# Optimization experiments

Measured on AMD Instinct MI355X. Metric: run time of the kernel, lower is better.

Reference implementation:

```python
import jax, jax.numpy as jnp
import numpy as np

HIDDEN = 2048
EXPERTS = 8
INTER = 1024
TOP_K = 2
AUX_LOSS_WEIGHT = 0.01
TOKENS = 8192


def setup_inputs() -> dict:
    key = jax.random.key(0)
    k_x, k_g, k_w1, k_w2 = jax.random.split(key, 4)
    x = jax.random.normal(k_x, (TOKENS, HIDDEN), dtype=jnp.float32)
    # nn.Linear(hidden, experts, bias=False): weight is [E, H], applied as x @ W^T
    gate_w = jax.random.normal(k_g, (EXPERTS, HIDDEN), dtype=jnp.float32) * 0.02
    w1 = jax.random.normal(k_w1, (EXPERTS, HIDDEN, INTER), dtype=jnp.float32) * 0.02
    w2 = jax.random.normal(k_w2, (EXPERTS, INTER, HIDDEN), dtype=jnp.float32) * 0.02
    return {"x": x, "gate_w": gate_w, "w1": w1, "w2": w2}


def _moe_forward(x, gate_w, w1, w2):
    E = gate_w.shape[0]
    logits = x @ gate_w.T                              # [T, E]
    probs = jax.nn.softmax(logits, axis=-1)            # [T, E]
    topk_w, topk_idx = jax.lax.top_k(probs, TOP_K)     # [T, K]
    topk_w = topk_w / jnp.sum(topk_w, axis=-1, keepdims=True)

    # load-balancing aux loss: E * sum_e f_e * P_e
    one_hot = jax.nn.one_hot(topk_idx, E, dtype=probs.dtype)   # [T, K, E]
    f = jnp.mean(jnp.sum(one_hot, axis=1), axis=0)             # fraction of tokens per expert
    P = jnp.mean(probs, axis=0)                                # mean router prob per expert
    aux_loss = AUX_LOSS_WEIGHT * E * jnp.sum(f * P)

    # grouped expert MLP (dense-over-experts formulation, same math as
    # permute -> grouped GEMM -> unpermute):
    h = jnp.einsum('th,ehi->tei', x, w1)               # [T, E, I]
    h = jax.nn.gelu(h)
    y = jnp.einsum('tei,eih->teh', h, w2)              # [T, E, H]

    # combine: gather each token's top-k expert outputs and weight them
    y_sel = jnp.take_along_axis(y, topk_idx[:, :, None], axis=1)  # [T, K, H]
    out = jnp.sum(y_sel * topk_w[:, :, None], axis=1)             # [T, H]
    return out, aux_loss


def reference(x, gate_w, w1, w2):
    return _moe_forward(x, gate_w, w1, w2)
```

## Files before the change

kernel.cpp:

```cpp
#include <hip/hip_runtime.h>
#include <hip/hip_fp16.h>
#include <cmath>

#define T_TOKENS 8192
#define HID 2048
#define NEXP 8
#define INTERM 1024
#define GATE_NB 2048
#define MAX_TT 136
#define GEMM_NB 512

typedef _Float16 f16x8 __attribute__((ext_vector_type(8)));
typedef _Float16 f16x4 __attribute__((ext_vector_type(4)));
typedef float f32x4 __attribute__((ext_vector_type(4)));

static __device__ __forceinline__ float gelu_tanh(float v) {
    return 0.5f * v * (1.0f + tanhf(0.79788456080286535588f * (v + 0.044715f * v * v * v)));
}

static __device__ __forceinline__ void glds16(const void* g, void* l) {
    __builtin_amdgcn_global_load_lds((const __attribute__((address_space(1))) void*)g,
                                     (__attribute__((address_space(3))) void*)l, 16, 0, 0);
}

static __device__ __forceinline__ f16x8 lds_read(const _Float16* base, int row, int chunk) {
    int phys = chunk ^ (row & 7);
    return *reinterpret_cast<const f16x8*>(
        reinterpret_cast<const char*>(base) + row * 128 + phys * 16);
}

__global__ __launch_bounds__(256) void tconv_kernel(const float* __restrict__ in,
                                                    _Float16* __restrict__ out,
                                                    int R, int C) {
    __shared__ float t[32][33];
    int z = blockIdx.z;
    int r0 = blockIdx.y * 32, c0 = blockIdx.x * 32;
    int tid = threadIdx.x;
    int r = tid >> 3, c4 = (tid & 7) * 4;
    const float4 v = *reinterpret_cast<const float4*>(&in[((size_t)z * R + (r0 + r)) * C + c0 + c4]);
    t[r][c4 + 0] = v.x; t[r][c4 + 1] = v.y; t[r][c4 + 2] = v.z; t[r][c4 + 3] = v.w;
    __syncthreads();
    int oc = tid >> 3;
    int or4 = (tid & 7) * 4;
    f16x4 o;
    o[0] = (_Float16)t[or4 + 0][oc];
    o[1] = (_Float16)t[or4 + 1][oc];
    o[2] = (_Float16)t[or4 + 2][oc];
    o[3] = (_Float16)t[or4 + 3][oc];
    *reinterpret_cast<f16x4*>(&out[((size_t)z * C + (c0 + oc)) * R + r0 + or4]) = o;
}

__global__ __launch_bounds__(256) void gate_kernel(const float* __restrict__ x,
                                                   const float* __restrict__ gw,
                                                   _Float16* __restrict__ xh,
                                                   int* __restrict__ tk_idx, float* __restrict__ tk_w,
                                                   int* __restrict__ part_cnt,
                                                   double* __restrict__ part_sumP) {
    __shared__ double sds[4][NEXP];
    __shared__ int sci[4][NEXP];
    int w = threadIdx.x >> 6;
    int lane = threadIdx.x & 63;
    int t = blockIdx.x * 4 + w;

    const float4* xr = (const float4*)(x + (size_t)t * HID);
    _Float16* xo = xh + (size_t)t * HID;
    double acc[NEXP];
#pragma unroll
    for (int e = 0; e < NEXP; e++) acc[e] = 0.0;
#pragma unroll
    for (int i = 0; i < HID / 256; i++) {
        float4 xv = xr[i * 64 + lane];
        f16x4 h;
        h[0] = (_Float16)xv.x; h[1] = (_Float16)xv.y;
        h[2] = (_Float16)xv.z; h[3] = (_Float16)xv.w;
        *reinterpret_cast<f16x4*>(xo + i * 256 + lane * 4) = h;
#pragma unroll
        for (int e = 0; e < NEXP; e++) {
            float4 gv = ((const float4*)(gw + (size_t)e * HID))[i * 64 + lane];
            acc[e] += (double)xv.x * (double)gv.x + (double)xv.y * (double)gv.y
                    + (double)xv.z * (double)gv.z + (double)xv.w * (double)gv.w;
        }
    }
#pragma unroll
    for (int e = 0; e < NEXP; e++) {
#pragma unroll
        for (int off = 32; off > 0; off >>= 1) acc[e] += __shfl_xor(acc[e], off, 64);
    }
    double mx = acc[0];
#pragma unroll
    for (int e = 1; e < NEXP; e++) mx = acc[e] > mx ? acc[e] : mx;
    double ex[NEXP];
    double sum = 0.0;
#pragma unroll
    for (int e = 0; e < NEXP; e++) { ex[e] = exp(acc[e] - mx); sum += ex[e]; }
    int i0 = 0;
#pragma unroll
    for (int e = 1; e < NEXP; e++) if (ex[e] > ex[i0]) i0 = e;
    int i1 = (i0 == 0) ? 1 : 0;
#pragma unroll
    for (int e = 0; e < NEXP; e++) if (e != i0 && ex[e] > ex[i1]) i1 = e;
    double p0 = ex[i0], p1 = ex[i1];
    double t2 = p0 + p1;
    if (lane == 0) {
        tk_idx[2 * t] = i0; tk_idx[2 * t + 1] = i1;
        tk_w[2 * t] = (float)(p0 / t2); tk_w[2 * t + 1] = (float)(p1 / t2);
#pragma unroll
        for (int e = 0; e < NEXP; e++) {
            sds[w][e] = ex[e] / sum;
            sci[w][e] = (e == i0 ? 1 : 0) + (e == i1 ? 1 : 0);
        }
    }
    __syncthreads();
    if (threadIdx.x < NEXP) {
        int e = threadIdx.x;
        part_sumP[e * GATE_NB + blockIdx.x] = sds[0][e] + sds[1][e] + sds[2][e] + sds[3][e];
        part_cnt[e * GATE_NB + blockIdx.x]  = sci[0][e] + sci[1][e] + sci[2][e] + sci[3][e];
    }
}

__global__ __launch_bounds__(256) void finalize_kernel(const int* __restrict__ part_cnt,
                                                       const double* __restrict__ part_sumP,
                                                       int* __restrict__ cnt, int* __restrict__ offs,
                                                       int* __restrict__ cursor,
                                                       int* __restrict__ ttab,
                                                       float* __restrict__ aux_out) {
    __shared__ double swv[4];
    __shared__ int cwv[4];
    __shared__ double sE[NEXP];
    __shared__ int cE[NEXP];
    int w = threadIdx.x >> 6;
    int lane = threadIdx.x & 63;
    for (int e = 0; e < NEXP; e++) {
        double s = 0.0; int c = 0;
        for (int j = threadIdx.x; j < GATE_NB; j += 256) {
            s += part_sumP[e * GATE_NB + j];
            c += part_cnt[e * GATE_NB + j];
        }
#pragma unroll
        for (int off = 32; off > 0; off >>= 1) {
            s += __shfl_xor(s, off, 64);
            c += __shfl_xor(c, off, 64);
        }
        if (lane == 0) { swv[w] = s; cwv[w] = c; }
        __syncthreads();
        if (threadIdx.x == 0) {
            sE[e] = swv[0] + swv[1] + swv[2] + swv[3];
            cE[e] = cwv[0] + cwv[1] + cwv[2] + cwv[3];
        }
        __syncthreads();
    }
    if (threadIdx.x == 0) {
        int off = 0;
        double aux = 0.0;
        int idx = 0;
#pragma unroll
        for (int e = 0; e < NEXP; e++) {
            cnt[e] = cE[e];
            offs[e] = off;
            off += cE[e];
            cursor[e] = 0;
            aux += ((double)cE[e] / (double)T_TOKENS) * (sE[e] / (double)T_TOKENS);
            int mt = (cE[e] + 127) >> 7;
            for (int m = 0; m < mt; m++) ttab[idx++] = (e << 16) | m;
        }
        for (; idx < MAX_TT; idx++) ttab[idx] = -1;
        aux_out[0] = (float)(0.01 * (double)NEXP * aux);
    }
}

__global__ void scatter_kernel(const int* __restrict__ tk_idx, const float* __restrict__ tk_w,
                               const int* __restrict__ offs, int* __restrict__ cursor,
                               int* __restrict__ row_tok, float* __restrict__ row_w,
                               int* __restrict__ tok_row) {
    int t = blockIdx.x * blockDim.x + threadIdx.x;
    int lane = threadIdx.x & 63;
    unsigned long long below = (lane == 0) ? 0ull : ((~0ull) >> (64 - lane));
    for (int k = 0; k < 2; k++) {
        int e = tk_idx[2 * t + k];
        float wv = tk_w[2 * t + k];
        int pos = 0;
#pragma unroll
        for (int ee = 0; ee < NEXP; ee++) {
            unsigned long long m = __ballot(e == ee);
            if (e == ee) {
                int rank = (int)__popcll(m & below);
                int leader = (int)__ffsll((unsigned long long)m) - 1;
                int b = 0;
                if (lane == leader) b = atomicAdd(&cursor[ee], (int)__popcll(m));
                b = __shfl(b, leader, 64);
                pos = b + rank;
            }
        }
        int r = offs[e] + pos;
        row_tok[r] = t;
        row_w[r] = wv;
        tok_row[2 * t + k] = r;
    }
}

template<bool GATHER, bool GELU, int KTOT, int NX>
__global__ __launch_bounds__(256, 2) void gemm8_kernel(
    const _Float16* __restrict__ Aglob,
    const _Float16* __restrict__ Bglob,
    const int* __restrict__ cnt, const int* __restrict__ offs,
    const int* __restrict__ row_tok,
    const int* __restrict__ ttab,
    _Float16* __restrict__ Out, int Ncols)
{
    constexpr int NT = KTOT / 64;
    __shared__ __align__(16) _Float16 As[2][128][64];
    __shared__ __align__(16) _Float16 Bs[2][128][64];

    int tid = threadIdx.x;
    int w = tid >> 6, lane = tid & 63;
    int wr = w >> 1, wc = w & 1;
    int fr = lane & 15, fq = lane >> 4;

    int srow = tid >> 3;
    int lc = (tid & 7) ^ (srow & 7);

    _Float16* ldsA = &As[0][0][0] + w * 512;
    _Float16* ldsB = &Bs[0][0][0] + w * 512;

    for (int it = blockIdx.x; it < MAX_TT * NX; it += gridDim.x) {
        int ent = ttab[it / NX];
        if (ent < 0) continue;
        int e = ent >> 16;
        int m0 = (ent & 0xffff) << 7;
        int Ne = cnt[e];
        int base = offs[e];
        int n0 = (it & (NX - 1)) << 7;

        const _Float16* aS[4];
#pragma unroll
        for (int r = 0; r < 4; r++) {
            int ar = m0 + r * 32 + srow; if (ar >= Ne) ar = Ne - 1;
            int id = GATHER ? row_tok[base + ar] : (base + ar);
            aS[r] = Aglob + (size_t)id * KTOT + lc * 8;
        }
        const size_t bexp = (size_t)e * Ncols * KTOT;
        const _Float16* bS[4];
#pragma unroll
        for (int r = 0; r < 4; r++)
            bS[r] = Bglob + bexp + (size_t)(n0 + r * 32 + srow) * KTOT + lc * 8;

#define STAGE(S, KOFF) do {                                         \
        glds16(aS[0] + (KOFF), ldsA + (S) * 8192 + 0 * 2048);       \
        glds16(aS[1] + (KOFF), ldsA + (S) * 8192 + 1 * 2048);       \
        glds16(aS[2] + (KOFF), ldsA + (S) * 8192 + 2 * 2048);       \
        glds16(aS[3] + (KOFF), ldsA + (S) * 8192 + 3 * 2048);       \
        glds16(bS[0] + (KOFF), ldsB + (S) * 8192 + 0 * 2048);       \
        glds16(bS[1] + (KOFF), ldsB + (S) * 8192 + 1 * 2048);       \
        glds16(bS[2] + (KOFF), ldsB + (S) * 8192 + 2 * 2048);       \
        glds16(bS[3] + (KOFF), ldsB + (S) * 8192 + 3 * 2048);       \
    } while (0)

        f32x4 acc[4][4] = {};
        STAGE(0, 0);

        for (int j = 0; j < NT; ++j) {
            int slot = j & 1;
            const _Float16* Ab = &As[slot][0][0];
            const _Float16* Bb = &Bs[slot][0][0];
            if (j + 1 < NT) {
                STAGE(slot ^ 1, (j + 1) * 64);
                asm volatile("s_waitcnt vmcnt(8)" ::: "memory");
            } else {
                asm volatile("s_waitcnt vmcnt(0)" ::: "memory");
            }
            __builtin_amdgcn_s_barrier();

            f16x8 b_[4][2];
            {
                f16x8 a_[2][2];
#pragma unroll
                for (int i = 0; i < 2; i++)
#pragma unroll
                    for (int k = 0; k < 2; k++)
                        a_[i][k] = lds_read(Ab, wr * 64 + i * 16 + fr, k * 4 + fq);
#pragma unroll
                for (int jj = 0; jj < 4; jj++)
#pragma unroll
                    for (int k = 0; k < 2; k++)
                        b_[jj][k] = lds_read(Bb, wc * 64 + jj * 16 + fr, k * 4 + fq);
                asm volatile("s_waitcnt lgkmcnt(0)" ::: "memory");
                __builtin_amdgcn_s_setprio(1);
#pragma unroll
                for (int i = 0; i < 2; i++)
#pragma unroll
                    for (int jj = 0; jj < 4; jj++)
#pragma unroll
                        for (int k = 0; k < 2; k++)
                            acc[i][jj] = __builtin_amdgcn_mfma_f32_16x16x32_f16(
                                a_[i][k], b_[jj][k], acc[i][jj], 0, 0, 0);
                __builtin_amdgcn_s_setprio(0);
            }
            {
                f16x8 a_[2][2];
#pragma unroll
                for (int i = 0; i < 2; i++)
#pragma unroll
                    for (int k = 0; k < 2; k++)
                        a_[i][k] = lds_read(Ab, wr * 64 + (2 + i) * 16 + fr, k * 4 + fq);
                asm volatile("s_waitcnt lgkmcnt(0)" ::: "memory");
                __builtin_amdgcn_s_setprio(1);
#pragma unroll
                for (int i = 0; i < 2; i++)
#pragma unroll
                    for (int jj = 0; jj < 4; jj++)
#pragma unroll
                        for (int k = 0; k < 2; k++)
                            acc[2 + i][jj] = __builtin_amdgcn_mfma_f32_16x16x32_f16(
                                a_[i][k], b_[jj][k], acc[2 + i][jj], 0, 0, 0);
                __builtin_amdgcn_s_setprio(0);
            }
            __builtin_amdgcn_s_barrier();
        }
#undef STAGE

#pragma unroll
        for (int mi = 0; mi < 4; mi++) {
#pragma unroll
            for (int r = 0; r < 4; r++) {
                int row = m0 + wr * 64 + mi * 16 + fq * 4 + r;
                if (row < Ne) {
                    _Float16* dst = Out + (size_t)(base + row) * Ncols + n0 + wc * 64 + fr;
#pragma unroll
                    for (int ni = 0; ni < 4; ni++) {
                        float v = acc[mi][ni][r];
                        if (GELU) v = gelu_tanh(v);
                        dst[ni * 16] = (_Float16)v;
                    }
                }
            }
        }
    }
}

__global__ __launch_bounds__(256) void combine_kernel(const _Float16* __restrict__ y,
                                                      const int* __restrict__ tok_row,
                                                      const float* __restrict__ tk_w,
                                                      float* __restrict__ out) {
    int t = blockIdx.x;
    int c = threadIdx.x;
    int r0 = tok_row[2 * t], r1 = tok_row[2 * t + 1];
    float w0 = tk_w[2 * t], w1 = tk_w[2 * t + 1];
    f16x8 a = reinterpret_cast<const f16x8*>(y + (size_t)r0 * HID)[c];
    f16x8 b = reinterpret_cast<const f16x8*>(y + (size_t)r1 * HID)[c];
    float4 o0, o1;
    o0.x = w0 * (float)a[0] + w1 * (float)b[0];
    o0.y = w0 * (float)a[1] + w1 * (float)b[1];
    o0.z = w0 * (float)a[2] + w1 * (float)b[2];
    o0.w = w0 * (float)a[3] + w1 * (float)b[3];
    o1.x = w0 * (float)a[4] + w1 * (float)b[4];
    o1.y = w0 * (float)a[5] + w1 * (float)b[5];
    o1.z = w0 * (float)a[6] + w1 * (float)b[6];
    o1.w = w0 * (float)a[7] + w1 * (float)b[7];
    float4* dst = reinterpret_cast<float4*>(out + (size_t)t * HID + c * 8);
    dst[0] = o0;
    dst[1] = o1;
}

extern "C" void kernel_launch(void* const* d_in, const int* in_sizes, int n_in,
                              void* d_out, int out_size, void* d_ws, size_t ws_size,
                              hipStream_t stream) {
    const float* x  = (const float*)d_in[0];
    const float* gw = (const float*)d_in[1];
    const float* w1 = (const float*)d_in[2];
    const float* w2 = (const float*)d_in[3];
    float* out = (float*)d_out;
    char* ws = (char*)d_ws;

    int*    cnt       = (int*)(ws + 0);
    int*    cursor    = (int*)(ws + 64);
    int*    offs      = (int*)(ws + 128);
    int*    ttab      = (int*)(ws + 512);
    int*    part_cnt  = (int*)(ws + 4096);
    double* part_sumP = (double*)(ws + 131072);
    int*    row_tok   = (int*)(ws + 262144);
    float*  row_w     = (float*)(ws + 327680);
    int*    tk_idx    = (int*)(ws + 393216);
    float*  tk_w      = (float*)(ws + 458752);
    int*    tok_row   = (int*)(ws + 524288);
    const size_t OFF = 589824;
    _Float16* xh  = (_Float16*)(ws + OFF);
    _Float16* w1t = (_Float16*)(ws + OFF + (1ull << 25));
    _Float16* w2t = (_Float16*)(ws + OFF + (2ull << 25));
    _Float16* hh  = (_Float16*)(ws + OFF + (3ull << 25));
    _Float16* y   = (_Float16*)(ws + OFF);

    dim3 g1(INTERM / 32, HID / 32, NEXP);
    tconv_kernel<<<g1, 256, 0, stream>>>(w1, w1t, HID, INTERM);
    dim3 g2(HID / 32, INTERM / 32, NEXP);
    tconv_kernel<<<g2, 256, 0, stream>>>(w2, w2t, INTERM, HID);

    gate_kernel<<<GATE_NB, 256, 0, stream>>>(x, gw, xh, tk_idx, tk_w, part_cnt, part_sumP);
    finalize_kernel<<<1, 256, 0, stream>>>(part_cnt, part_sumP, cnt, offs, cursor, ttab,
                                           out + (size_t)T_TOKENS * HID);
    scatter_kernel<<<T_TOKENS / 256, 256, 0, stream>>>(tk_idx, tk_w, offs, cursor,
                                                       row_tok, row_w, tok_row);

    gemm8_kernel<true, true, HID, INTERM / 128>
        <<<GEMM_NB, 256, 0, stream>>>(xh, w1t, cnt, offs, row_tok, ttab, hh, INTERM);
    gemm8_kernel<false, false, INTERM, HID / 128>
        <<<GEMM_NB, 256, 0, stream>>>(hh, w2t, cnt, offs, row_tok, ttab, y, HID);

    combine_kernel<<<T_TOKENS, 256, 0, stream>>>(y, tok_row, tk_w, out);
}
```

Before: 409.5 us.

## Use 256x128 GEMM tiles with K=32 stages and per-XCD atomic work stealing

The expert GEMM tile grows from 128x128 to 256x128 with a K step of 32 (LDS rows are now 64 bytes with a new swizzle), so each B tile is reused across twice as many rows. The static strided tile loop becomes a dynamic scheduler: each block takes work from an atomic counter indexed by blockIdx&7, which is meant to keep an XCD's work contiguous and to skip empty tile-table entries. The finalize kernel now records the real tile count and zeroes the steal counters. The cost is more accumulator registers, a shallower K stage that means more barriers, and more padding waste on small experts.

```diff
diff --git a/kernel.cpp b/kernel.cpp
--- a/kernel.cpp
+++ b/kernel.cpp
@@ -23,10 +23,10 @@
                                      (__attribute__((address_space(3))) void*)l, 16, 0, 0);
 }
 
-static __device__ __forceinline__ f16x8 lds_read(const _Float16* base, int row, int chunk) {
-    int phys = chunk ^ (row & 7);
+static __device__ __forceinline__ f16x8 lds_read32(const _Float16* base, int row, int chunk) {
+    int phys = chunk ^ ((row >> 1) & 3);
     return *reinterpret_cast<const f16x8*>(
-        reinterpret_cast<const char*>(base) + row * 128 + phys * 16);
+        reinterpret_cast<const char*>(base) + row * 64 + phys * 16);
 }
 
 __global__ __launch_bounds__(256) void tconv_kernel(const float* __restrict__ in,
@@ -123,6 +123,8 @@
                                                        int* __restrict__ cnt, int* __restrict__ offs,
                                                        int* __restrict__ cursor,
                                                        int* __restrict__ ttab,
+                                                       int* __restrict__ nmt,
+                                                       int* __restrict__ steal,
                                                        float* __restrict__ aux_out) {
     __shared__ double swv[4];
     __shared__ int cwv[4];
@@ -160,10 +162,12 @@
             off += cE[e];
             cursor[e] = 0;
             aux += ((double)cE[e] / (double)T_TOKENS) * (sE[e] / (double)T_TOKENS);
-            int mt = (cE[e] + 127) >> 7;
+            int mt = (cE[e] + 255) >> 8;
             for (int m = 0; m < mt; m++) ttab[idx++] = (e << 16) | m;
         }
+        nmt[0] = idx;
         for (; idx < MAX_TT; idx++) ttab[idx] = -1;
+        for (int i = 0; i < 16; i++) steal[i] = 0;
         aux_out[0] = (float)(0.01 * (double)NEXP * aux);
     }
 }
@@ -199,63 +203,75 @@
 }
 
 template<bool GATHER, bool GELU, int KTOT, int NX>
-__global__ __launch_bounds__(256, 2) void gemm8_kernel(
+__global__ __launch_bounds__(256, 2) void gemm9_kernel(
     const _Float16* __restrict__ Aglob,
     const _Float16* __restrict__ Bglob,
     const int* __restrict__ cnt, const int* __restrict__ offs,
     const int* __restrict__ row_tok,
     const int* __restrict__ ttab,
+    const int* __restrict__ nmt,
+    int* __restrict__ steal,
     _Float16* __restrict__ Out, int Ncols)
 {
-    constexpr int NT = KTOT / 64;
-    __shared__ __align__(16) _Float16 As[2][128][64];
-    __shared__ __align__(16) _Float16 Bs[2][128][64];
+    constexpr int NT = KTOT / 32;
+    __shared__ __align__(16) _Float16 As[2][256][32];
+    __shared__ __align__(16) _Float16 Bs[2][128][32];
+    __shared__ int s_it;
 
     int tid = threadIdx.x;
     int w = tid >> 6, lane = tid & 63;
     int wr = w >> 1, wc = w & 1;
     int fr = lane & 15, fq = lane >> 4;
 
-    int srow = tid >> 3;
-    int lc = (tid & 7) ^ (srow & 7);
-
-    _Float16* ldsA = &As[0][0][0] + w * 512;
-    _Float16* ldsB = &Bs[0][0][0] + w * 512;
-
-    for (int it = blockIdx.x; it < MAX_TT * NX; it += gridDim.x) {
+    int n_items = nmt[0] * NX;
+    int chunk = (n_items + 7) >> 3;
+    int xcd = blockIdx.x & 7;
+
+    int lrow = lane >> 2;
+    int lc = (lane & 3) ^ ((lane >> 3) & 3);
+
+    _Float16* ldsA = &As[0][0][0] + (w * 64) * 32;
+    _Float16* ldsB = &Bs[0][0][0] + (w * 32) * 32;
+
+    for (;;) {
+        __syncthreads();
+        if (tid == 0) s_it = atomicAdd(&steal[xcd], 1);
+        __syncthreads();
+        int i = s_it;
+        if (i >= chunk) break;
+        int it = xcd * chunk + i;
+        if (it >= n_items) break;
+
         int ent = ttab[it / NX];
-        if (ent < 0) continue;
         int e = ent >> 16;
-        int m0 = (ent & 0xffff) << 7;
+        int m0 = (ent & 0xffff) << 8;
         int Ne = cnt[e];
         int base = offs[e];
         int n0 = (it & (NX - 1)) << 7;
 
         const _Float16* aS[4];
 #pragma unroll
-        for (int r = 0; r < 4; r++) {
-            int ar = m0 + r * 32 + srow; if (ar >= Ne) ar = Ne - 1;
+        for (int g = 0; g < 4; g++) {
+            int ar = m0 + w * 64 + g * 16 + lrow; if (ar >= Ne) ar = Ne - 1;
             int id = GATHER ? row_tok[base + ar] : (base + ar);
-            aS[r] = Aglob + (size_t)id * KTOT + lc * 8;
+            aS[g] = Aglob + (size_t)id * KTOT + lc * 8;
         }
         const size_t bexp = (size_t)e * Ncols * KTOT;
-        const _Float16* bS[4];
-#pragma unroll
-        for (int r = 0; r < 4; r++)
-            bS[r] = Bglob + bexp + (size_t)(n0 + r * 32 + srow) * KTOT + lc * 8;
-
-#define STAGE(S, KOFF) do {                                         \
-        glds16(aS[0] + (KOFF), ldsA + (S) * 8192 + 0 * 2048);       \
-        glds16(aS[1] + (KOFF), ldsA + (S) * 8192 + 1 * 2048);       \
-        glds16(aS[2] + (KOFF), ldsA + (S) * 8192 + 2 * 2048);       \
-        glds16(aS[3] + (KOFF), ldsA + (S) * 8192 + 3 * 2048);       \
-        glds16(bS[0] + (KOFF), ldsB + (S) * 8192 + 0 * 2048);       \
-        glds16(bS[1] + (KOFF), ldsB + (S) * 8192 + 1 * 2048);       \
-        glds16(bS[2] + (KOFF), ldsB + (S) * 8192 + 2 * 2048);       \
-        glds16(bS[3] + (KOFF), ldsB + (S) * 8192 + 3 * 2048);       \
+        const _Float16* bS[2];
+#pragma unroll
+        for (int g = 0; g < 2; g++)
+            bS[g] = Bglob + bexp + (size_t)(n0 + w * 32 + g * 16 + lrow) * KTOT + lc * 8;
+
+#define STAGE(S, KOFF) do {                                     \
+        glds16(aS[0] + (KOFF), ldsA + (S) * 8192 + 0 * 512);    \
+        glds16(aS[1] + (KOFF), ldsA + (S) * 8192 + 1 * 512);    \
+        glds16(aS[2] + (KOFF), ldsA + (S) * 8192 + 2 * 512);    \
+        glds16(aS[3] + (KOFF), ldsA + (S) * 8192 + 3 * 512);    \
+        glds16(bS[0] + (KOFF), ldsB + (S) * 4096 + 0 * 512);    \
+        glds16(bS[1] + (KOFF), ldsB + (S) * 4096 + 1 * 512);    \
     } while (0)
 
-        f32x4 acc[4][4] = {};
+        f32x4 acc[8][4] = {};
         STAGE(0, 0);
 
         for (int j = 0; j < NT; ++j) {
@@ -263,55 +279,45 @@
             const _Float16* Ab = &As[slot][0][0];
             const _Float16* Bb = &Bs[slot][0][0];
             if (j + 1 < NT) {
-                STAGE(slot ^ 1, (j + 1) * 64);
-                asm volatile("s_waitcnt vmcnt(8)" ::: "memory");
+                STAGE(slot ^ 1, (j + 1) * 32);
+                asm volatile("s_waitcnt vmcnt(6)" ::: "memory");
             } else {
                 asm volatile("s_waitcnt vmcnt(0)" ::: "memory");
             }
             __builtin_amdgcn_s_barrier();
 
-            f16x8 b_[4][2];
+            f16x8 b_[4];
+#pragma unroll
+            for (int jj = 0; jj < 4; jj++)
+                b_[jj] = lds_read32(Bb, wc * 64 + jj * 16 + fr, fq);
             {
-                f16x8 a_[2][2];
-#pragma unroll
-                for (int i = 0; i < 2; i++)
-#pragma unroll
-                    for (int k = 0; k < 2; k++)
-                        a_[i][k] = lds_read(Ab, wr * 64 + i * 16 + fr, k * 4 + fq);
-#pragma unroll
-                for (int jj = 0; jj < 4; jj++)
-#pragma unroll
-                    for (int k = 0; k < 2; k++)
-                        b_[jj][k] = lds_read(Bb, wc * 64 + jj * 16 + fr, k * 4 + fq);
+                f16x8 a_[4];
+#pragma unroll
+                for (int ii = 0; ii < 4; ii++)
+                    a_[ii] = lds_read32(Ab, wr * 128 + ii * 16 + fr, fq);
                 asm volatile("s_waitcnt lgkmcnt(0)" ::: "memory");
                 __builtin_amdgcn_s_setprio(1);
 #pragma unroll
-                for (int i = 0; i < 2; i++)
+                for (int ii = 0; ii < 4; ii++)
 #pragma unroll
                     for (int jj = 0; jj < 4; jj++)
-#pragma unroll
-                        for (int k = 0; k < 2; k++)
-                            acc[i][jj] = __builtin_amdgcn_mfma_f32_16x16x32_f16(
-                                a_[i][k], b_[jj][k], acc[i][jj], 0, 0, 0);
+                        acc[ii][jj] = __builtin_amdgcn_mfma_f32_16x16x32_f16(
+                            a_[ii], b_[jj], acc[ii][jj], 0, 0, 0);
                 __builtin_amdgcn_s_setprio(0);
             }
             {
-                f16x8 a_[2][2];
-#pragma unroll
-                for (int i = 0; i < 2; i++)
-#pragma unroll
-                    for (int k = 0; k < 2; k++)
-                        a_[i][k] = lds_read(Ab, wr * 64 + (2 + i) * 16 + fr, k * 4 + fq);
+                f16x8 a_[4];
+#pragma unroll
+                for (int ii = 0; ii < 4; ii++)
+                    a_[ii] = lds_read32(Ab, wr * 128 + (4 + ii) * 16 + fr, fq);
                 asm volatile("s_waitcnt lgkmcnt(0)" ::: "memory");
                 __builtin_amdgcn_s_setprio(1);
 #pragma unroll
-                for (int i = 0; i < 2; i++)
+                for (int ii = 0; ii < 4; ii++)
 #pragma unroll
                     for (int jj = 0; jj < 4; jj++)
-#pragma unroll
-                        for (int k = 0; k < 2; k++)
-                            acc[2 + i][jj] = __builtin_amdgcn_mfma_f32_16x16x32_f16(
-                                a_[i][k], b_[jj][k], acc[2 + i][jj], 0, 0, 0);
+                        acc[4 + ii][jj] = __builtin_amdgcn_mfma_f32_16x16x32_f16(
+                            a_[ii], b_[jj], acc[4 + ii][jj], 0, 0, 0);
                 __builtin_amdgcn_s_setprio(0);
             }
             __builtin_amdgcn_s_barrier();
@@ -319,10 +325,10 @@
 #undef STAGE
 
 #pragma unroll
-        for (int mi = 0; mi < 4; mi++) {
+        for (int mi = 0; mi < 8; mi++) {
 #pragma unroll
             for (int r = 0; r < 4; r++) {
-                int row = m0 + wr * 64 + mi * 16 + fq * 4 + r;
+                int row = m0 + wr * 128 + mi * 16 + fq * 4 + r;
                 if (row < Ne) {
                     _Float16* dst = Out + (size_t)(base + row) * Ncols + n0 + wc * 64 + fr;
 #pragma unroll
@@ -374,6 +380,8 @@
     int*    cnt       = (int*)(ws + 0);
     int*    cursor    = (int*)(ws + 64);
     int*    offs      = (int*)(ws + 128);
+    int*    nmt       = (int*)(ws + 256);
+    int*    steal     = (int*)(ws + 320);
     int*    ttab      = (int*)(ws + 512);
     int*    part_cnt  = (int*)(ws + 4096);
     double* part_sumP = (double*)(ws + 131072);
@@ -396,14 +404,14 @@
 
     gate_kernel<<<GATE_NB, 256, 0, stream>>>(x, gw, xh, tk_idx, tk_w, part_cnt, part_sumP);
     finalize_kernel<<<1, 256, 0, stream>>>(part_cnt, part_sumP, cnt, offs, cursor, ttab,
-                                           out + (size_t)T_TOKENS * HID);
+                                           nmt, steal, out + (size_t)T_TOKENS * HID);
     scatter_kernel<<<T_TOKENS / 256, 256, 0, stream>>>(tk_idx, tk_w, offs, cursor,
                                                        row_tok, row_w, tok_row);
 
-    gemm8_kernel<true, true, HID, INTERM / 128>
-        <<<GEMM_NB, 256, 0, stream>>>(xh, w1t, cnt, offs, row_tok, ttab, hh, INTERM);
-    gemm8_kernel<false, false, INTERM, HID / 128>
-        <<<GEMM_NB, 256, 0, stream>>>(hh, w2t, cnt, offs, row_tok, ttab, y, HID);
+    gemm9_kernel<true, true, HID, INTERM / 128>
+        <<<GEMM_NB, 256, 0, stream>>>(xh, w1t, cnt, offs, row_tok, ttab, nmt, steal, hh, INTERM);
+    gemm9_kernel<false, false, INTERM, HID / 128>
+        <<<GEMM_NB, 256, 0, stream>>>(hh, w2t, cnt, offs, row_tok, ttab, nmt, steal + 8, y, HID);
 
     combine_kernel<<<T_TOKENS, 256, 0, stream>>>(y, tok_row, tk_w, out);
 }
```

Result: slower. 446.0 us (+8.9%).

## Schedule grouped GEMM tiles via per-XCD atomic work-stealing counters

Applied to the files above, without the earlier changes.

Replaces the static grid-stride loop over the padded tile table with dynamic tile fetching. Each block takes its next tile from an atomic counter belonging to its XCD, and the live tiles are split into eight contiguous chunks, one per XCD, so that L2 reuse of weights and activations stays local. Empty padded table entries are no longer visited. The cost is an atomic plus two block barriers per tile, and the scheme assumes blocks map to XCDs round-robin by blockIdx.

```diff
diff --git a/kernel.cpp b/kernel.cpp
--- a/kernel.cpp
+++ b/kernel.cpp
@@ -123,6 +123,8 @@
                                                        int* __restrict__ cnt, int* __restrict__ offs,
                                                        int* __restrict__ cursor,
                                                        int* __restrict__ ttab,
+                                                       int* __restrict__ nmt,
+                                                       int* __restrict__ steal,
                                                        float* __restrict__ aux_out) {
     __shared__ double swv[4];
     __shared__ int cwv[4];
@@ -163,7 +165,9 @@
             int mt = (cE[e] + 127) >> 7;
             for (int m = 0; m < mt; m++) ttab[idx++] = (e << 16) | m;
         }
+        nmt[0] = idx;
         for (; idx < MAX_TT; idx++) ttab[idx] = -1;
+        for (int i = 0; i < 16; i++) steal[i] = 0;
         aux_out[0] = (float)(0.01 * (double)NEXP * aux);
     }
 }
@@ -205,26 +209,40 @@
     const int* __restrict__ cnt, const int* __restrict__ offs,
     const int* __restrict__ row_tok,
     const int* __restrict__ ttab,
+    const int* __restrict__ nmt,
+    int* __restrict__ steal,
     _Float16* __restrict__ Out, int Ncols)
 {
     constexpr int NT = KTOT / 64;
     __shared__ __align__(16) _Float16 As[2][128][64];
     __shared__ __align__(16) _Float16 Bs[2][128][64];
+    __shared__ int s_it;
 
     int tid = threadIdx.x;
     int w = tid >> 6, lane = tid & 63;
     int wr = w >> 1, wc = w & 1;
     int fr = lane & 15, fq = lane >> 4;
 
+    int n_items = nmt[0] * NX;
+    int chunk = (n_items + 7) >> 3;
+    int xcd = blockIdx.x & 7;
+
     int srow = tid >> 3;
     int lc = (tid & 7) ^ (srow & 7);
 
     _Float16* ldsA = &As[0][0][0] + w * 512;
     _Float16* ldsB = &Bs[0][0][0] + w * 512;
 
-    for (int it = blockIdx.x; it < MAX_TT * NX; it += gridDim.x) {
+    for (;;) {
+        __syncthreads();
+        if (tid == 0) s_it = atomicAdd(&steal[xcd], 1);
+        __syncthreads();
+        int i = s_it;
+        if (i >= chunk) break;
+        int it = xcd * chunk + i;
+        if (it >= n_items) break;
+
         int ent = ttab[it / NX];
-        if (ent < 0) continue;
         int e = ent >> 16;
         int m0 = (ent & 0xffff) << 7;
         int Ne = cnt[e];
@@ -274,10 +292,10 @@
             {
                 f16x8 a_[2][2];
 #pragma unroll
-                for (int i = 0; i < 2; i++)
+                for (int i2 = 0; i2 < 2; i2++)
 #pragma unroll
                     for (int k = 0; k < 2; k++)
-                        a_[i][k] = lds_read(Ab, wr * 64 + i * 16 + fr, k * 4 + fq);
+                        a_[i2][k] = lds_read(Ab, wr * 64 + i2 * 16 + fr, k * 4 + fq);
 #pragma unroll
                 for (int jj = 0; jj < 4; jj++)
 #pragma unroll
@@ -286,32 +304,32 @@
                 asm volatile("s_waitcnt lgkmcnt(0)" ::: "memory");
                 __builtin_amdgcn_s_setprio(1);
 #pragma unroll
-                for (int i = 0; i < 2; i++)
+                for (int i2 = 0; i2 < 2; i2++)
 #pragma unroll
                     for (int jj = 0; jj < 4; jj++)
 #pragma unroll
                         for (int k = 0; k < 2; k++)
-                            acc[i][jj] = __builtin_amdgcn_mfma_f32_16x16x32_f16(
-                                a_[i][k], b_[jj][k], acc[i][jj], 0, 0, 0);
+                            acc[i2][jj] = __builtin_amdgcn_mfma_f32_16x16x32_f16(
+                                a_[i2][k], b_[jj][k], acc[i2][jj], 0, 0, 0);
                 __builtin_amdgcn_s_setprio(0);
             }
             {
                 f16x8 a_[2][2];
 #pragma unroll
-                for (int i = 0; i < 2; i++)
+                for (int i2 = 0; i2 < 2; i2++)
 #pragma unroll
                     for (int k = 0; k < 2; k++)
-                        a_[i][k] = lds_read(Ab, wr * 64 + (2 + i) * 16 + fr, k * 4 + fq);
+                        a_[i2][k] = lds_read(Ab, wr * 64 + (2 + i2) * 16 + fr, k * 4 + fq);
                 asm volatile("s_waitcnt lgkmcnt(0)" ::: "memory");
                 __builtin_amdgcn_s_setprio(1);
 #pragma unroll
-                for (int i = 0; i < 2; i++)
+                for (int i2 = 0; i2 < 2; i2++)
 #pragma unroll
                     for (int jj = 0; jj < 4; jj++)
 #pragma unroll
                         for (int k = 0; k < 2; k++)
-                            acc[2 + i][jj] = __builtin_amdgcn_mfma_f32_16x16x32_f16(
-                                a_[i][k], b_[jj][k], acc[2 + i][jj], 0, 0, 0);
+                            acc[2 + i2][jj] = __builtin_amdgcn_mfma_f32_16x16x32_f16(
+                                a_[i2][k], b_[jj][k], acc[2 + i2][jj], 0, 0, 0);
                 __builtin_amdgcn_s_setprio(0);
             }
             __builtin_amdgcn_s_barrier();
@@ -374,6 +392,8 @@
     int*    cnt       = (int*)(ws + 0);
     int*    cursor    = (int*)(ws + 64);
     int*    offs      = (int*)(ws + 128);
+    int*    nmt       = (int*)(ws + 256);
+    int*    steal     = (int*)(ws + 320);
     int*    ttab      = (int*)(ws + 512);
     int*    part_cnt  = (int*)(ws + 4096);
     double* part_sumP = (double*)(ws + 131072);
@@ -396,14 +416,14 @@
 
     gate_kernel<<<GATE_NB, 256, 0, stream>>>(x, gw, xh, tk_idx, tk_w, part_cnt, part_sumP);
     finalize_kernel<<<1, 256, 0, stream>>>(part_cnt, part_sumP, cnt, offs, cursor, ttab,
-                                           out + (size_t)T_TOKENS * HID);
+                                           nmt, steal, out + (size_t)T_TOKENS * HID);
     scatter_kernel<<<T_TOKENS / 256, 256, 0, stream>>>(tk_idx, tk_w, offs, cursor,
                                                        row_tok, row_w, tok_row);
 
     gemm8_kernel<true, true, HID, INTERM / 128>
-        <<<GEMM_NB, 256, 0, stream>>>(xh, w1t, cnt, offs, row_tok, ttab, hh, INTERM);
+        <<<GEMM_NB, 256, 0, stream>>>(xh, w1t, cnt, offs, row_tok, ttab, nmt, steal, hh, INTERM);
     gemm8_kernel<false, false, INTERM, HID / 128>
-        <<<GEMM_NB, 256, 0, stream>>>(hh, w2t, cnt, offs, row_tok, ttab, y, HID);
+        <<<GEMM_NB, 256, 0, stream>>>(hh, w2t, cnt, offs, row_tok, ttab, nmt, steal + 8, y, HID);
 
     combine_kernel<<<T_TOKENS, 256, 0, stream>>>(y, tok_row, tk_w, out);
 }
```

Measured after the change: 411.5 us. About the same (+0.5%).
